# Kernel tuning notes

Measured on AMD Instinct MI355X. Metric: run time of the kernel, lower is better.

The kernel has to match this reference:

```python
import jax, jax.numpy as jnp
import numpy as np
from jax import lax

NEG = -1e16  # value used by masked_fill in the original
DN = ('NCHW', 'OIHW', 'NCHW')


def _time_block(X, w1, b1, w2, b2, w3, b3):
    # X: [B, N, T, C] -> conv over time with kernel (1,3), VALID -> [B, N, T-2, O]
    x = jnp.transpose(X, (0, 3, 1, 2))  # [B, C, N, T]
    conv = lambda w, b: lax.conv_general_dilated(x, w, (1, 1), 'VALID', dimension_numbers=DN) + b[None, :, None, None]
    temp = conv(w1, b1) + jax.nn.sigmoid(conv(w2, b2))
    out = jax.nn.relu(temp + conv(w3, b3))
    return jnp.transpose(out, (0, 2, 3, 1))  # [B, N, T-2, O]


def _gat_single(x, graph, W, b):
    # x: [B, N, C]; W: [D, C]; b: [D]
    h = jnp.einsum('bnc,dc->bnd', x, W)
    s = jnp.einsum('bnd,bmd->bnm', h, h) * graph[None]
    s = jnp.where(s == 0, NEG, s)
    a = jax.nn.softmax(s, axis=-1)
    return jnp.einsum('bnm,bmd->bnd', a, h) + b


def _gat_multihead(x, graph, Wh, bh):
    # x: [B, N, C]; Wh: [H, D, C]; bh: [H, D] -> [B, N, H*D] (head-major concat, matching torch.cat)
    h = jnp.einsum('bnc,hdc->bhnd', x, Wh)
    s = jnp.einsum('bhnd,bhmd->bhnm', h, h) * graph[None, None]
    s = jnp.where(s == 0, NEG, s)
    a = jax.nn.softmax(s, axis=-1)
    o = jnp.einsum('bhnm,bhmd->bhnd', a, h) + bh[None, :, None, :]
    B, H, N, D = o.shape
    return jnp.transpose(o, (0, 2, 1, 3)).reshape(B, N, H * D)


def setup_inputs() -> dict:
    key = jax.random.key(0)
    ks = jax.random.split(key, 12)
    B, N, T, C = 2, 4096, 5, 192
    hid, out_c, H = 64, 64, 4
    inp = {
        'flow': jax.random.normal(ks[0], (B, N, T, C), jnp.float32),
        'graph': jax.random.randint(ks[1], (N, N), 0, 2).astype(jnp.float32),
        'tb_w1': jax.random.normal(ks[2], (hid, C, 1, 3), jnp.float32) * 0.1,
        'tb_b1': jax.random.normal(ks[3], (hid,), jnp.float32) * 0.1,
        'tb_w2': jax.random.normal(ks[4], (hid, C, 1, 3), jnp.float32) * 0.1,
        'tb_b2': jax.random.normal(ks[5], (hid,), jnp.float32) * 0.1,
        'tb_w3': jax.random.normal(ks[6], (hid, C, 1, 3), jnp.float32) * 0.1,
        'tb_b3': jax.random.normal(ks[7], (hid,), jnp.float32) * 0.1,
        'Wh': jax.random.normal(ks[8], (H, hid, C), jnp.float32) * 0.1,
        'bh': jax.random.normal(ks[9], (H, hid), jnp.float32) * 0.1,
        'Wo': jax.random.normal(ks[10], (out_c, hid * H), jnp.float32) * 0.1,
        'bo': jax.random.normal(ks[11], (out_c,), jnp.float32) * 0.1,
    }
    return inp


def reference(flow, graph, tb_w1, tb_b1, tb_w2, tb_b2, tb_w3, tb_b3, Wh, bh, Wo, bo):
    B, N = flow.shape[0], flow.shape[1]
    t1 = _time_block(flow, tb_w1, tb_b1, tb_w2, tb_b2, tb_w3, tb_b3)  # [B, N, T-2, hid]
    x = t1.reshape(B, N, -1)  # [B, N, (T-2)*hid]
    x = jax.nn.leaky_relu(_gat_multihead(x, graph, Wh, bh), negative_slope=0.01)
    x = jax.nn.leaky_relu(_gat_single(x, graph, Wo, bo), negative_slope=0.01)
    return x[:, :, None, :]  # [B, N, 1, out_c]
```

## Files before the change

### kernel.cpp

```cpp
#include <hip/hip_runtime.h>
#include <math.h>

#define N_NODES 4096

typedef unsigned short u16;
typedef unsigned int u32;

typedef __attribute__((ext_vector_type(8))) short bfrag;
typedef __attribute__((ext_vector_type(4))) float f4;

__device__ __forceinline__ u16 f2bf(float x) {
    union { float f; u32 u; } v; v.f = x;
    u32 r = (v.u + 0x7FFFu + ((v.u >> 16) & 1u)) >> 16;
    return (u16)r;
}
__device__ __forceinline__ float bf2f(u16 b) {
    union { float f; u32 u; } v; v.u = ((u32)b) << 16; return v.f;
}
__device__ __forceinline__ u32 cvtpk(float a, float b) {
    u32 r;
    asm("v_cvt_pk_bf16_f32 %0, %1, %2" : "=v"(r) : "v"(a), "v"(b));
    return r;
}
__device__ __forceinline__ float u2f(u32 u) {
    union { u32 u; float f; } v; v.u = u; return v.f;
}
__device__ __forceinline__ float fexp2(float x) {
    float r;
    asm("v_exp_f32 %0, %1" : "=v"(r) : "v"(x));
    return r;
}

#define LOG2E 1.4426950408889634f

__global__ __launch_bounds__(256) void wprep_kernel(
    const float* __restrict__ w1, const float* __restrict__ w2,
    const float* __restrict__ w3,
    u16* __restrict__ w_hi, u16* __restrict__ w_mid, u16* __restrict__ w_lo)
{
    int idx = blockIdx.x * 256 + threadIdx.x;
    if (idx >= 192 * 576) return;
    int col = idx / 576, k = idx % 576;
    int conv = col >> 6, o = col & 63;
    int kk = k / 192, c = k % 192;
    const float* w = (conv == 0) ? w1 : (conv == 1 ? w2 : w3);
    float v = w[(o * 192 + c) * 3 + kk];
    u16 h = f2bf(v);   float r1 = v - bf2f(h);
    u16 m = f2bf(r1);  float r2 = r1 - bf2f(m);
    u16 lo = f2bf(r2);
    int kc = k >> 6, rem = k & 63, j = rem >> 3, e = rem & 7;
    int pos = col * 576 + kc * 64 + ((j ^ (col & 7)) << 3) + e;
    w_hi[pos] = h;
    w_mid[pos] = m;
    w_lo[pos] = lo;
}

__global__ __launch_bounds__(512) void timeblock_mfma_kernel(
    const float* __restrict__ flow,
    const u16* __restrict__ w_hi, const u16* __restrict__ w_mid,
    const u16* __restrict__ w_lo,
    const float* __restrict__ b1, const float* __restrict__ b2,
    const float* __restrict__ b3, float* __restrict__ x1)
{
    __shared__ __align__(16) u16 As[3][128 * 64];
    __shared__ __align__(16) u16 Bs[3][192 * 64];

    const int tid = threadIdx.x;
    const int wv = tid >> 6, l = tid & 63;
    const int ln15 = l & 15, ln16 = l >> 4;
    const int wr = wv >> 1, wc = wv & 1;
    const int nodebase = blockIdx.x * 128;
    const int t = blockIdx.y;

    f4 acc[2][6];
#pragma unroll
    for (int rq = 0; rq < 2; ++rq)
#pragma unroll
        for (int nt = 0; nt < 6; ++nt) {
            acc[rq][nt][0] = 0.f; acc[rq][nt][1] = 0.f;
            acc[rq][nt][2] = 0.f; acc[rq][nt][3] = 0.f;
        }

    for (int kc = 0; kc < 9; ++kc) {
        __syncthreads();

#pragma unroll
        for (int u = tid; u < 1024; u += 512) {
            int r = u >> 3, j = u & 7;
            const float* srcp = flow + (size_t)(nodebase + r) * 960 + t * 192 + kc * 64 + j * 8;
            float4 f0 = *(const float4*)srcp;
            float4 f1 = *(const float4*)(srcp + 4);
            float fv[8] = { f0.x, f0.y, f0.z, f0.w, f1.x, f1.y, f1.z, f1.w };
            union { uint4 q; u16 a[8]; } uh, um, ul;
#pragma unroll
            for (int e = 0; e < 8; ++e) {
                u16 h = f2bf(fv[e]);   float r1 = fv[e] - bf2f(h);
                u16 m = f2bf(r1);      float r2 = r1 - bf2f(m);
                uh.a[e] = h; um.a[e] = m; ul.a[e] = f2bf(r2);
            }
            int pos = r * 64 + ((j ^ (r & 7)) << 3);
            *(uint4*)&As[0][pos] = uh.q;
            *(uint4*)&As[1][pos] = um.q;
            *(uint4*)&As[2][pos] = ul.q;
        }

#pragma unroll
        for (int arr = 0; arr < 3; ++arr) {
            const u16* wsrc = (arr == 0) ? w_hi : (arr == 1 ? w_mid : w_lo);
#pragma unroll
            for (int i = 0; i < 3; ++i) {
                int colg = wv * 24 + i * 8;
                const u16* srcp = wsrc + (size_t)(colg + (l >> 3)) * 576 + kc * 64 + (l & 7) * 8;
                u16* dstp = &Bs[arr][colg * 64];
                __builtin_amdgcn_global_load_lds(
                    (const __attribute__((address_space(1))) u32*)srcp,
                    (__attribute__((address_space(3))) u32*)dstp, 16, 0, 0);
            }
        }

        __syncthreads();

        bfrag af[2][3][2];
#pragma unroll
        for (int rq = 0; rq < 2; ++rq) {
            int arow = wr * 32 + rq * 16 + ln15;
#pragma unroll
            for (int ks = 0; ks < 2; ++ks) {
                int idx = arow * 64 + (((ks * 4 + ln16) ^ (arow & 7)) << 3);
                af[rq][0][ks] = *(const bfrag*)&As[0][idx];
                af[rq][1][ks] = *(const bfrag*)&As[1][idx];
                af[rq][2][ks] = *(const bfrag*)&As[2][idx];
            }
        }

#pragma unroll
        for (int cv = 0; cv < 3; ++cv) {
#pragma unroll
            for (int ntj = 0; ntj < 2; ++ntj) {
                int col = cv * 64 + wc * 32 + ntj * 16 + ln15;
                int nt = cv * 2 + ntj;
#pragma unroll
                for (int ks = 0; ks < 2; ++ks) {
                    int idx = col * 64 + (((ks * 4 + ln16) ^ (col & 7)) << 3);
                    bfrag bh = *(const bfrag*)&Bs[0][idx];
                    bfrag bm = *(const bfrag*)&Bs[1][idx];
                    bfrag bl = *(const bfrag*)&Bs[2][idx];
#pragma unroll
                    for (int rq = 0; rq < 2; ++rq) {
                        f4 a = acc[rq][nt];
                        a = __builtin_amdgcn_mfma_f32_16x16x32_bf16(af[rq][0][ks], bh, a, 0, 0, 0);
                        a = __builtin_amdgcn_mfma_f32_16x16x32_bf16(af[rq][0][ks], bm, a, 0, 0, 0);
                        a = __builtin_amdgcn_mfma_f32_16x16x32_bf16(af[rq][1][ks], bh, a, 0, 0, 0);
                        a = __builtin_amdgcn_mfma_f32_16x16x32_bf16(af[rq][0][ks], bl, a, 0, 0, 0);
                        a = __builtin_amdgcn_mfma_f32_16x16x32_bf16(af[rq][2][ks], bh, a, 0, 0, 0);
                        a = __builtin_amdgcn_mfma_f32_16x16x32_bf16(af[rq][1][ks], bm, a, 0, 0, 0);
                        acc[rq][nt] = a;
                    }
                }
            }
        }
    }

#pragma unroll
    for (int rq = 0; rq < 2; ++rq) {
#pragma unroll
        for (int ntj = 0; ntj < 2; ++ntj) {
            int o = wc * 32 + ntj * 16 + ln15;
            float bb1 = b1[o], bb2 = b2[o], bb3 = b3[o];
#pragma unroll
            for (int rg = 0; rg < 4; ++rg) {
                int node = nodebase + wr * 32 + rq * 16 + ln16 * 4 + rg;
                float c1 = acc[rq][0 * 2 + ntj][rg] + bb1;
                float c2 = acc[rq][1 * 2 + ntj][rg] + bb2;
                float c3 = acc[rq][2 * 2 + ntj][rg] + bb3;
                float sg = 1.0f / (1.0f + __expf(-c2));
                float v = c1 + sg + c3;
                x1[(size_t)node * 192 + t * 64 + o] = v > 0.f ? v : 0.f;
            }
        }
    }
}

__global__ __launch_bounds__(256) void linear64_split_kernel(
    const float* __restrict__ in, const float* __restrict__ W,
    u16* __restrict__ h_hi, u16* __restrict__ h_lo,
    u16* __restrict__ hTb_hi, u16* __restrict__ hTb_lo,
    int C, int H)
{
    __shared__ float xs[64][68];
    __shared__ float wsm[64][68];
    const int tid = threadIdx.x;
    const int g = blockIdx.y;
    const int rowbase = blockIdx.x * 64;
    const int rgrp = tid >> 4, cgrp = tid & 15;

    float acc[4][4] = {};
    for (int c0 = 0; c0 < C; c0 += 64) {
        __syncthreads();
        for (int i = tid; i < 4096; i += 256) {
            int r = i >> 6, cc = i & 63;
            xs[r][cc]  = in[(size_t)(rowbase + r) * C + c0 + cc];
            wsm[r][cc] = W[(size_t)(g * 64 + r) * C + c0 + cc];
        }
        __syncthreads();
        for (int cc = 0; cc < 64; cc += 4) {
            float4 xv[4], wv[4];
#pragma unroll
            for (int i = 0; i < 4; ++i)
                xv[i] = *reinterpret_cast<const float4*>(&xs[4 * rgrp + i][cc]);
#pragma unroll
            for (int j = 0; j < 4; ++j)
                wv[j] = *reinterpret_cast<const float4*>(&wsm[4 * cgrp + j][cc]);
#pragma unroll
            for (int i = 0; i < 4; ++i) {
#pragma unroll
                for (int j = 0; j < 4; ++j) {
                    acc[i][j] += xv[i].x * wv[j].x + xv[i].y * wv[j].y
                               + xv[i].z * wv[j].z + xv[i].w * wv[j].w;
                }
            }
        }
    }

    u16 hi[4][4], lo[4][4];
#pragma unroll
    for (int i = 0; i < 4; ++i)
#pragma unroll
        for (int j = 0; j < 4; ++j) {
            float a = acc[i][j];
            u16 h = f2bf(a);
            hi[i][j] = h;
            lo[i][j] = f2bf(a - bf2f(h));
        }

    const int b = rowbase >> 12;
    const size_t mapb = (size_t)(b * H + g) * (4096 * 64);

#pragma unroll
    for (int i = 0; i < 4; ++i) {
        int n = (rowbase & 4095) + 4 * rgrp + i;
        ushort4 vh = { hi[i][0], hi[i][1], hi[i][2], hi[i][3] };
        ushort4 vl = { lo[i][0], lo[i][1], lo[i][2], lo[i][3] };
        *(ushort4*)&h_hi[mapb + (size_t)n * 64 + 4 * cgrp] = vh;
        *(ushort4*)&h_lo[mapb + (size_t)n * 64 + 4 * cgrp] = vl;
    }
    {
        int n0 = (rowbase & 4095) + 4 * rgrp;
        size_t tb = mapb + ((size_t)(n0 >> 6) * 64) * 64;
#pragma unroll
        for (int j = 0; j < 4; ++j) {
            int d = 4 * cgrp + j;
            ushort4 vh = { hi[0][j], hi[1][j], hi[2][j], hi[3][j] };
            ushort4 vl = { lo[0][j], lo[1][j], lo[2][j], lo[3][j] };
            *(ushort4*)&hTb_hi[tb + (size_t)d * 64 + (n0 & 63)] = vh;
            *(ushort4*)&hTb_lo[tb + (size_t)d * 64 + (n0 & 63)] = vl;
        }
    }
}

__global__ __launch_bounds__(256) void flash_mfma_kernel(
    const u16* __restrict__ h_hi, const u16* __restrict__ h_lo,
    const u16* __restrict__ hTb_hi, const u16* __restrict__ hTb_lo,
    const float* __restrict__ graph, const float* __restrict__ bias,
    float* __restrict__ out, int H, int rstride,
    int ntiles, int nch, int mode, float* __restrict__ pO, float* __restrict__ pml)
{
    __shared__ __align__(16) u16 hcs[2][4][4096];

    const int tid = threadIdx.x;
    const int wv = tid >> 6;
    const int l = tid & 63;
    const int ln15 = l & 15, ln16 = l >> 4;
    const int bx = blockIdx.y;
    const int by = bx / nch;
    const int chunk = bx - by * nch;
    const int t0 = chunk * ntiles;
    const int bb = by / H, head = by - bb * H;
    const size_t mapb = (size_t)by * (4096 * 64);
    const int rowbase = blockIdx.x * 64;

    const int arow = rowbase + wv * 16 + ln15;
    bfrag ahi[2], alo[2];
#pragma unroll
    for (int ks = 0; ks < 2; ++ks) {
        ahi[ks] = *(const bfrag*)(h_hi + mapb + (size_t)arow * 64 + ks * 32 + ln16 * 8);
        alo[ks] = *(const bfrag*)(h_lo + mapb + (size_t)arow * 64 + ks * 32 + ln16 * 8);
    }

    const u16* gA = (wv == 0 ? h_hi : wv == 1 ? h_lo : wv == 2 ? hTb_hi : hTb_lo) + mapb;
    const int lrow = l >> 3;
    const int stoff = lrow * 64 + (((l & 7) ^ lrow) << 3);

#define STAGE(T, BUF)                                                          \
    {                                                                          \
        const u16* srcp = gA + (size_t)(T) * 4096 + stoff;                     \
        u16* dstp = &hcs[BUF][wv][0];                                          \
        _Pragma("unroll")                                                      \
        for (int i_ = 0; i_ < 8; ++i_)                                         \
            __builtin_amdgcn_global_load_lds(                                  \
                (const __attribute__((address_space(1))) u32*)(srcp + i_ * 512), \
                (__attribute__((address_space(3))) u32*)(dstp + i_ * 512),     \
                16, 0, 0);                                                     \
    }

    const float* grow = graph + (size_t)(rowbase + wv * 16 + ln15) * 4096 + ln16 * 4;

    float m_ = -3.0e38f, l_ = 0.f;
    f4 acco[4];
#pragma unroll
    for (int i = 0; i < 4; ++i) {
        acco[i][0] = 0.f; acco[i][1] = 0.f; acco[i][2] = 0.f; acco[i][3] = 0.f;
    }

    STAGE(t0, 0);
    float4 grC[4], grN[4];
#pragma unroll
    for (int cb = 0; cb < 4; ++cb)
        grC[cb] = *(const float4*)(grow + (size_t)t0 * 64 + cb * 16);

    const int srcA = ln15 + ((((ln16 << 1)) & 3) << 4);
    const int srcB = ln15 + ((((ln16 << 1) + 1) & 3) << 4);
    const bool hi2 = (ln16 & 2) != 0;

    for (int tt = 0; tt < ntiles; ++tt) {
        const int t = t0 + tt;
        const int cur = tt & 1;

        __syncthreads();

        if (tt + 1 < ntiles) {
            STAGE(t + 1, cur ^ 1);
#pragma unroll
            for (int cb = 0; cb < 4; ++cb)
                grN[cb] = *(const float4*)(grow + (size_t)(t + 1) * 64 + cb * 16);
        }

        __builtin_amdgcn_s_setprio(1);
        f4 accs[4];
#pragma unroll
        for (int cb = 0; cb < 4; ++cb) {
            f4 a; a[0] = 0.f; a[1] = 0.f; a[2] = 0.f; a[3] = 0.f;
#pragma unroll
            for (int ks = 0; ks < 2; ++ks) {
                int c = cb * 16 + ln15;
                int idx = c * 64 + (((ks * 4 + ln16) * 8) ^ ((c & 7) << 3));
                bfrag bhi = *(const bfrag*)&hcs[cur][0][idx];
                bfrag blo = *(const bfrag*)&hcs[cur][1][idx];
                a = __builtin_amdgcn_mfma_f32_16x16x32_bf16(bhi, ahi[ks], a, 0, 0, 0);
                a = __builtin_amdgcn_mfma_f32_16x16x32_bf16(bhi, alo[ks], a, 0, 0, 0);
                a = __builtin_amdgcn_mfma_f32_16x16x32_bf16(blo, ahi[ks], a, 0, 0, 0);
            }
            accs[cb] = a;
        }
        __builtin_amdgcn_s_setprio(0);

        float p[4][4];
#pragma unroll
        for (int cb = 0; cb < 4; ++cb) {
            p[cb][0] = accs[cb][0] + fmaf(grC[cb].x, 1e16f, -1e16f);
            p[cb][1] = accs[cb][1] + fmaf(grC[cb].y, 1e16f, -1e16f);
            p[cb][2] = accs[cb][2] + fmaf(grC[cb].z, 1e16f, -1e16f);
            p[cb][3] = accs[cb][3] + fmaf(grC[cb].w, 1e16f, -1e16f);
        }

        float tm = fmaxf(fmaxf(p[0][0], p[0][1]), fmaxf(p[0][2], p[0][3]));
#pragma unroll
        for (int cb = 1; cb < 4; ++cb)
            tm = fmaxf(tm, fmaxf(fmaxf(p[cb][0], p[cb][1]), fmaxf(p[cb][2], p[cb][3])));
        tm = fmaxf(tm, __shfl_xor(tm, 16));
        tm = fmaxf(tm, __shfl_xor(tm, 32));

        const bool anyup = __any(tm > m_);
        float mn, corr;
        if (anyup) {
            mn = fmaxf(m_, tm);
            corr = fexp2((m_ - mn) * LOG2E);
        } else {
            mn = m_;
            corr = 1.0f;
        }
        const float c0 = -mn * LOG2E;

        float rs = 0.f;
#pragma unroll
        for (int cb = 0; cb < 4; ++cb) {
            p[cb][0] = fexp2(fmaf(p[cb][0], LOG2E, c0));
            p[cb][1] = fexp2(fmaf(p[cb][1], LOG2E, c0));
            p[cb][2] = fexp2(fmaf(p[cb][2], LOG2E, c0));
            p[cb][3] = fexp2(fmaf(p[cb][3], LOG2E, c0));
            rs += (p[cb][0] + p[cb][1]) + (p[cb][2] + p[cb][3]);
        }
        rs += __shfl_xor(rs, 16);
        rs += __shfl_xor(rs, 32);
        l_ = l_ * corr + rs;
        m_ = mn;

        if (anyup) {
            float corr4[4];
#pragma unroll
            for (int rg = 0; rg < 4; ++rg)
                corr4[rg] = __shfl(corr, ln16 * 4 + rg);
#pragma unroll
            for (int nb = 0; nb < 4; ++nb) {
                acco[nb][0] *= corr4[0]; acco[nb][1] *= corr4[1];
                acco[nb][2] *= corr4[2]; acco[nb][3] *= corr4[3];
            }
        }

        u32 Uh[4][2], Ul[4][2];
#pragma unroll
        for (int cb = 0; cb < 4; ++cb) {
            u32 uh0 = cvtpk(p[cb][0], p[cb][1]);
            u32 uh1 = cvtpk(p[cb][2], p[cb][3]);
            float h0 = u2f(uh0 << 16), h1 = u2f(uh0 & 0xffff0000u);
            float h2 = u2f(uh1 << 16), h3 = u2f(uh1 & 0xffff0000u);
            Uh[cb][0] = uh0; Uh[cb][1] = uh1;
            Ul[cb][0] = cvtpk(p[cb][0] - h0, p[cb][1] - h1);
            Ul[cb][1] = cvtpk(p[cb][2] - h2, p[cb][3] - h3);
        }

        bfrag pfh[2], pfl[2];
#pragma unroll
        for (int ks = 0; ks < 2; ++ks) {
            u32 w0a = (u32)__shfl((int)Uh[2 * ks + 0][0], srcA);
            u32 w0b = (u32)__shfl((int)Uh[2 * ks + 1][0], srcA);
            u32 w1a = (u32)__shfl((int)Uh[2 * ks + 0][1], srcA);
            u32 w1b = (u32)__shfl((int)Uh[2 * ks + 1][1], srcA);
            u32 w2a = (u32)__shfl((int)Uh[2 * ks + 0][0], srcB);
            u32 w2b = (u32)__shfl((int)Uh[2 * ks + 1][0], srcB);
            u32 w3a = (u32)__shfl((int)Uh[2 * ks + 0][1], srcB);
            u32 w3b = (u32)__shfl((int)Uh[2 * ks + 1][1], srcB);
            union { uint4 q; bfrag f; } ch;
            ch.q.x = hi2 ? w0b : w0a; ch.q.y = hi2 ? w1b : w1a;
            ch.q.z = hi2 ? w2b : w2a; ch.q.w = hi2 ? w3b : w3a;
            pfh[ks] = ch.f;

            u32 v0a = (u32)__shfl((int)Ul[2 * ks + 0][0], srcA);
            u32 v0b = (u32)__shfl((int)Ul[2 * ks + 1][0], srcA);
            u32 v1a = (u32)__shfl((int)Ul[2 * ks + 0][1], srcA);
            u32 v1b = (u32)__shfl((int)Ul[2 * ks + 1][1], srcA);
            u32 v2a = (u32)__shfl((int)Ul[2 * ks + 0][0], srcB);
            u32 v2b = (u32)__shfl((int)Ul[2 * ks + 1][0], srcB);
            u32 v3a = (u32)__shfl((int)Ul[2 * ks + 0][1], srcB);
            u32 v3b = (u32)__shfl((int)Ul[2 * ks + 1][1], srcB);
            union { uint4 q; bfrag f; } cl;
            cl.q.x = hi2 ? v0b : v0a; cl.q.y = hi2 ? v1b : v1a;
            cl.q.z = hi2 ? v2b : v2a; cl.q.w = hi2 ? v3b : v3a;
            pfl[ks] = cl.f;
        }

        __builtin_amdgcn_s_setprio(1);
#pragma unroll
        for (int nb = 0; nb < 4; ++nb) {
#pragma unroll
            for (int ks = 0; ks < 2; ++ks) {
                int nr = nb * 16 + ln15;
                int idx = nr * 64 + (((ks * 4 + ln16) * 8) ^ ((nr & 7) << 3));
                bfrag vhi = *(const bfrag*)&hcs[cur][2][idx];
                bfrag vlo = *(const bfrag*)&hcs[cur][3][idx];
                acco[nb] = __builtin_amdgcn_mfma_f32_16x16x32_bf16(pfh[ks], vhi, acco[nb], 0, 0, 0);
                acco[nb] = __builtin_amdgcn_mfma_f32_16x16x32_bf16(pfh[ks], vlo, acco[nb], 0, 0, 0);
                acco[nb] = __builtin_amdgcn_mfma_f32_16x16x32_bf16(pfl[ks], vhi, acco[nb], 0, 0, 0);
            }
        }
        __builtin_amdgcn_s_setprio(0);

        if (tt + 1 < ntiles) {
#pragma unroll
            for (int cb = 0; cb < 4; ++cb)
                grC[cb] = grN[cb];
        }
    }
#undef STAGE

    if (mode == 0) {
        float l4[4];
#pragma unroll
        for (int rg = 0; rg < 4; ++rg)
            l4[rg] = __shfl(l_, ln16 * 4 + rg);

        const float* bv = bias + head * 64;
#pragma unroll
        for (int rg = 0; rg < 4; ++rg) {
            int row = rowbase + wv * 16 + ln16 * 4 + rg;
            float inv = 1.0f / l4[rg];
#pragma unroll
            for (int nb = 0; nb < 4; ++nb) {
                float v = acco[nb][rg] * inv + bv[nb * 16 + ln15];
                v = v > 0.f ? v : 0.01f * v;
                out[(size_t)(bb * N_NODES + row) * rstride + head * 64 + nb * 16 + ln15] = v;
            }
        }
    } else {
        int row = rowbase + wv * 16 + ln15;
        if (ln16 == 0) {
            size_t mi = (((size_t)(by * nch + chunk)) * 4096 + row) * 2;
            pml[mi] = m_;
            pml[mi + 1] = l_;
        }
#pragma unroll
        for (int rg = 0; rg < 4; ++rg) {
            int row2 = rowbase + wv * 16 + ln16 * 4 + rg;
            size_t ob = (((size_t)(by * nch + chunk)) * 4096 + row2) * 64;
#pragma unroll
            for (int nb = 0; nb < 4; ++nb)
                pO[ob + nb * 16 + ln15] = acco[nb][rg];
        }
    }
}

__global__ __launch_bounds__(256) void merge_kernel(
    const float* __restrict__ pO, const float* __restrict__ pml,
    const float* __restrict__ bias, float* __restrict__ out)
{
    int idx = blockIdx.x * 256 + threadIdx.x;
    int feat = idx & 63;
    int row = (idx >> 6) & 4095;
    int map = idx >> 18;

    float mv[4], lv[4];
    float M = -3.0e38f;
#pragma unroll
    for (int c = 0; c < 4; ++c) {
        size_t mi = (((size_t)map * 4 + c) * 4096 + row) * 2;
        mv[c] = pml[mi];
        lv[c] = pml[mi + 1];
        M = fmaxf(M, mv[c]);
    }
    float den = 0.f, num = 0.f;
#pragma unroll
    for (int c = 0; c < 4; ++c) {
        float e = __expf(mv[c] - M);
        den += e * lv[c];
        num += e * pO[(((size_t)map * 4 + c) * 4096 + row) * 64 + feat];
    }
    float v = num / den + bias[feat];
    v = v > 0.f ? v : 0.01f * v;
    out[((size_t)map * 4096 + row) * 64 + feat] = v;
}

extern "C" void kernel_launch(void* const* d_in, const int* in_sizes, int n_in,
                              void* d_out, int out_size, void* d_ws, size_t ws_size,
                              hipStream_t stream)
{
    const float* flow = (const float*)d_in[0];
    const float* graph = (const float*)d_in[1];
    const float* w1 = (const float*)d_in[2];
    const float* b1 = (const float*)d_in[3];
    const float* w2 = (const float*)d_in[4];
    const float* b2 = (const float*)d_in[5];
    const float* w3 = (const float*)d_in[6];
    const float* b3 = (const float*)d_in[7];
    const float* Wh = (const float*)d_in[8];
    const float* bh = (const float*)d_in[9];
    const float* Wo = (const float*)d_in[10];
    const float* bo = (const float*)d_in[11];

    char* ws = (char*)d_ws;
    u16* wc_hi  = (u16*)ws;
    u16* wc_mid = wc_hi + (size_t)192 * 576;
    u16* wc_lo  = wc_mid + (size_t)192 * 576;

    u16* h1_hi  = (u16*)ws;
    u16* h1_lo  = h1_hi + (size_t)8 * 4096 * 64;
    u16* h1T_hi = h1_lo + (size_t)8 * 4096 * 64;
    u16* h1T_lo = h1T_hi + (size_t)8 * 4096 * 64;
    u16* h2_hi  = (u16*)ws;
    u16* h2_lo  = h2_hi + (size_t)2 * 4096 * 64;
    u16* h2T_hi = h2_lo + (size_t)2 * 4096 * 64;
    u16* h2T_lo = h2T_hi + (size_t)2 * 4096 * 64;
    float* pml  = (float*)(ws + (size_t)6 * 1024 * 1024);
    float* xreg = (float*)(ws + (size_t)4 * 8 * 4096 * 64 * 2);
    float* x1 = xreg;
    float* x2 = xreg;
    float* pO = xreg;
    float* outp = (float*)d_out;

    hipLaunchKernelGGL(wprep_kernel, dim3(432), dim3(256), 0, stream,
                       w1, w2, w3, wc_hi, wc_mid, wc_lo);
    hipLaunchKernelGGL(timeblock_mfma_kernel, dim3(64, 3), dim3(512), 0, stream,
                       flow, wc_hi, wc_mid, wc_lo, b1, b2, b3, x1);
    hipLaunchKernelGGL(linear64_split_kernel, dim3(128, 4), dim3(256), 0, stream,
                       x1, Wh, h1_hi, h1_lo, h1T_hi, h1T_lo, 192, 4);
    hipLaunchKernelGGL(flash_mfma_kernel, dim3(64, 8), dim3(256), 0, stream,
                       h1_hi, h1_lo, h1T_hi, h1T_lo, graph, bh, x2, 4, 256,
                       64, 1, 0, (float*)nullptr, (float*)nullptr);
    hipLaunchKernelGGL(linear64_split_kernel, dim3(128, 1), dim3(256), 0, stream,
                       x2, Wo, h2_hi, h2_lo, h2T_hi, h2T_lo, 256, 1);
    hipLaunchKernelGGL(flash_mfma_kernel, dim3(64, 8), dim3(256), 0, stream,
                       h2_hi, h2_lo, h2T_hi, h2T_lo, graph, bo, (float*)nullptr, 1, 64,
                       16, 4, 1, pO, pml);
    hipLaunchKernelGGL(merge_kernel, dim3(2048), dim3(256), 0, stream,
                       pO, pml, bo, outp);
}
```

Baseline: 316.5 us.

## Single-buffer V tiles in LDS and load them just in time

Splits the shared staging buffer into double-buffered K tiles and a single-buffered V tile. V for the current tile is now loaded at the start of each iteration and consumed after an extra barrier placed after the softmax. This cuts LDS per block from 64KB to 48KB, which is meant to let more blocks share a CU. The cost is a second __syncthreads per iteration and V load latency that is only hidden behind the QK and softmax phase rather than a full iteration.

```diff
diff --git a/kernel.cpp b/kernel.cpp
--- a/kernel.cpp
+++ b/kernel.cpp
@@ -265,7 +265,8 @@
     float* __restrict__ out, int H, int rstride,
     int ntiles, int nch, int mode, float* __restrict__ pO, float* __restrict__ pml)
 {
-    __shared__ __align__(16) u16 hcs[2][4][4096];
+    __shared__ __align__(16) u16 Ks[2][2][4096];
+    __shared__ __align__(16) u16 Vs[2][4096];
 
     const int tid = threadIdx.x;
     const int wv = tid >> 6;
@@ -291,10 +292,10 @@
     const int lrow = l >> 3;
     const int stoff = lrow * 64 + (((l & 7) ^ lrow) << 3);
 
-#define STAGE(T, BUF)                                                          \
-    {                                                                          \
+#define STAGE_K(T, BUF)                                                        \
+    if (wv < 2) {                                                              \
         const u16* srcp = gA + (size_t)(T) * 4096 + stoff;                     \
-        u16* dstp = &hcs[BUF][wv][0];                                          \
+        u16* dstp = &Ks[BUF][wv][0];                                           \
         _Pragma("unroll")                                                      \
         for (int i_ = 0; i_ < 8; ++i_)                                         \
             __builtin_amdgcn_global_load_lds(                                  \
@@ -302,6 +303,17 @@
                 (__attribute__((address_space(3))) u32*)(dstp + i_ * 512),     \
                 16, 0, 0);                                                     \
     }
+#define STAGE_V(T)                                                             \
+    if (wv >= 2) {                                                             \
+        const u16* srcp = gA + (size_t)(T) * 4096 + stoff;                     \
+        u16* dstp = &Vs[wv - 2][0];                                            \
+        _Pragma("unroll")                                                      \
+        for (int i_ = 0; i_ < 8; ++i_)                                         \
+            __builtin_amdgcn_global_load_lds(                                  \
+                (const __attribute__((address_space(1))) u32*)(srcp + i_ * 512), \
+                (__attribute__((address_space(3))) u32*)(dstp + i_ * 512),     \
+                16, 0, 0);                                                     \
+    }
 
     const float* grow = graph + (size_t)(rowbase + wv * 16 + ln15) * 4096 + ln16 * 4;
 
@@ -312,7 +324,7 @@
         acco[i][0] = 0.f; acco[i][1] = 0.f; acco[i][2] = 0.f; acco[i][3] = 0.f;
     }
 
-    STAGE(t0, 0);
+    STAGE_K(t0, 0);
     float4 grC[4], grN[4];
 #pragma unroll
     for (int cb = 0; cb < 4; ++cb)
@@ -328,8 +340,9 @@
 
         __syncthreads();
 
+        STAGE_V(t);
         if (tt + 1 < ntiles) {
-            STAGE(t + 1, cur ^ 1);
+            STAGE_K(t + 1, cur ^ 1);
 #pragma unroll
             for (int cb = 0; cb < 4; ++cb)
                 grN[cb] = *(const float4*)(grow + (size_t)(t + 1) * 64 + cb * 16);
@@ -344,8 +357,8 @@
             for (int ks = 0; ks < 2; ++ks) {
                 int c = cb * 16 + ln15;
                 int idx = c * 64 + (((ks * 4 + ln16) * 8) ^ ((c & 7) << 3));
-                bfrag bhi = *(const bfrag*)&hcs[cur][0][idx];
-                bfrag blo = *(const bfrag*)&hcs[cur][1][idx];
+                bfrag bhi = *(const bfrag*)&Ks[cur][0][idx];
+                bfrag blo = *(const bfrag*)&Ks[cur][1][idx];
                 a = __builtin_amdgcn_mfma_f32_16x16x32_bf16(bhi, ahi[ks], a, 0, 0, 0);
                 a = __builtin_amdgcn_mfma_f32_16x16x32_bf16(bhi, alo[ks], a, 0, 0, 0);
                 a = __builtin_amdgcn_mfma_f32_16x16x32_bf16(blo, ahi[ks], a, 0, 0, 0);
@@ -449,6 +462,8 @@
             pfl[ks] = cl.f;
         }
 
+        __syncthreads();
+
         __builtin_amdgcn_s_setprio(1);
 #pragma unroll
         for (int nb = 0; nb < 4; ++nb) {
@@ -456,8 +471,8 @@
             for (int ks = 0; ks < 2; ++ks) {
                 int nr = nb * 16 + ln15;
                 int idx = nr * 64 + (((ks * 4 + ln16) * 8) ^ ((nr & 7) << 3));
-                bfrag vhi = *(const bfrag*)&hcs[cur][2][idx];
-                bfrag vlo = *(const bfrag*)&hcs[cur][3][idx];
+                bfrag vhi = *(const bfrag*)&Vs[0][idx];
+                bfrag vlo = *(const bfrag*)&Vs[1][idx];
                 acco[nb] = __builtin_amdgcn_mfma_f32_16x16x32_bf16(pfh[ks], vhi, acco[nb], 0, 0, 0);
                 acco[nb] = __builtin_amdgcn_mfma_f32_16x16x32_bf16(pfh[ks], vlo, acco[nb], 0, 0, 0);
                 acco[nb] = __builtin_amdgcn_mfma_f32_16x16x32_bf16(pfl[ks], vhi, acco[nb], 0, 0, 0);
@@ -471,7 +486,8 @@
                 grC[cb] = grN[cb];
         }
     }
-#undef STAGE
+#undef STAGE_K
+#undef STAGE_V
 
     if (mode == 0) {
         float l4[4];
```

Result: no change. 313.7 us (-0.9%).
